# Optimization experiments

Measured on AMD Instinct MI355X. Metric: run time of the kernel, lower is better.

The kernel has to match this reference:

```python
import jax, jax.numpy as jnp
import numpy as np

NEG_SLOPE = 0.2
K_L = 0.5
K_G = 0.5
TEMP_G = 1e-3


def _leaky(v):
    return jnp.where(v >= 0, v, NEG_SLOPE * v)


def _topk_row_mask(scores, keep):
    # scores: [n, n, h]; torch.topk(dim=0) -> indices [keep, n] per head,
    # then head_mask[indices, :] = 1 selects whole ROWS (any column hit).
    n = scores.shape[0]
    s = jnp.transpose(scores, (1, 2, 0))        # [n_cols, h, n_rows]
    _, idx = jax.lax.top_k(s, keep)             # [n_cols, h, keep]

    def per_head(idx_h):                        # idx_h: [n_cols, keep]
        return jnp.zeros((n,), scores.dtype).at[idx_h.reshape(-1)].set(1.0)

    rows = jax.vmap(per_head, in_axes=1, out_axes=0)(idx)  # [h, n_rows]
    return jnp.transpose(rows)[:, None, :]      # [n_rows, 1, h] broadcast over cols


def setup_inputs() -> dict:
    key = jax.random.key(0)
    ks = jax.random.split(key, 8)
    n, in_f, feat_dim = 1024, 256, 128
    H, F = 4, 64                                # n_heads, n_hidden (out_features=256)
    feats = jax.random.normal(ks[0], (n, feat_dim), dtype=jnp.float32)
    x = jax.random.normal(ks[1], (n, in_f), dtype=jnp.float32)
    adj = jax.random.randint(ks[2], (n, n, 1), 0, 2).astype(jnp.int32)
    sc = 0.05
    W_l = jax.random.normal(ks[3], (in_f, H * F), dtype=jnp.float32) * sc
    W_r = jax.random.normal(ks[4], (in_f, H * F), dtype=jnp.float32) * sc
    attn_w = jax.random.normal(ks[5], (F,), dtype=jnp.float32) * sc
    W_delta = jax.random.normal(ks[6], (2 * F, F), dtype=jnp.float32) * sc
    b_delta = jnp.zeros((F,), dtype=jnp.float32)
    return {"feats": feats, "x": x, "adj": adj, "W_l": W_l, "W_r": W_r,
            "attn_w": attn_w, "W_delta": W_delta, "b_delta": b_delta}


def reference(feats, x, adj, W_l, W_r, attn_w, W_delta, b_delta):
    n = x.shape[0]
    F = attn_w.shape[0]
    H = W_l.shape[1] // F
    g_l = (x @ W_l).reshape(n, H, F)
    g_r = (x @ W_r).reshape(n, H, F)
    # g_sum[i, j] = g_l[j] + g_r[i]  (repeat vs repeat_interleave ordering)
    g_sum = g_r[:, None, :, :] + g_l[None, :, :, :]          # [n, n, H, F]
    e = jnp.einsum('ijhf,f->ijh', _leaky(g_sum), attn_w)     # [n, n, H]

    mask_adj = adj > 0                                        # [n, n, 1]
    a_l = jax.nn.softmax(jnp.where(mask_adj, e, -jnp.inf), axis=1)
    a_1nd = a_l * mask_adj.astype(e.dtype)

    keep_l = int(n * (1.0 - K_L))
    a_filt = a_1nd * _topk_row_mask(a_1nd, keep_l)
    attn_local = jnp.einsum('ijh,jhf->ihf', a_filt, g_r)     # [n, H, F]

    omega = jax.nn.softmax(e, axis=1)
    fn = (feats - feats.min(axis=0)) / (feats.max(axis=0) - feats.min(axis=0))
    fn = jnp.where(jnp.isnan(fn), 0.0, fn)
    g_rn = (g_r - g_r.min(axis=0)) / (g_r.max(axis=0) - g_r.min(axis=0))
    nf = jnp.linalg.norm(fn, axis=1)                          # [n] (index j)
    ng = jnp.linalg.norm(g_rn, axis=2)                        # [n, H] (index i)
    alpha = jax.nn.softmax(jnp.abs(nf[None, :, None] - ng[:, None, :]), axis=1)
    gamma = 0.5 * (omega + (1.0 - alpha))

    keep_g = int(n * (1.0 - K_G))
    gf = gamma * _topk_row_mask(gamma, keep_g)
    gf = jax.nn.softmax(jnp.where(gf == 0, 1e-10, gf) / TEMP_G, axis=1)
    attn_global = jnp.einsum('ijh,jhf->ihf', gf, g_r)         # [n, H, F]

    inter = _leaky(jnp.concatenate([attn_local, attn_global], axis=2) @ W_delta + b_delta)
    delta = jax.nn.softmax(inter, axis=1)                     # softmax over heads (torch dim=1)
    attn_res = delta * attn_local + (1.0 - delta) * attn_global
    return attn_res.reshape(n, H * F)
```

## Files before the change

kernel.cpp:

```cpp
#include <hip/hip_runtime.h>
#include <cstdint>
#include <cstddef>

#define N 1024
#define HN 4
#define FDIM 64
#define KSEL 512
#define FLT_MAX_ 3.402823466e+38f

__device__ __forceinline__ float wred_sum(float v){
#pragma unroll
  for(int o=32;o>0;o>>=1) v += __shfl_down(v,o,64);
  return v;
}
__device__ __forceinline__ float wred_max(float v){
#pragma unroll
  for(int o=32;o>0;o>>=1) v = fmaxf(v,__shfl_down(v,o,64));
  return v;
}
__device__ __forceinline__ float bred_sum(float v, float* scr){
  int t=threadIdx.x;
  v = wred_sum(v);
  __syncthreads();
  if((t&63)==0) scr[t>>6]=v;
  __syncthreads();
  return (scr[0]+scr[1])+(scr[2]+scr[3]);
}
__device__ __forceinline__ float bred_max(float v, float* scr){
  int t=threadIdx.x;
  v = wred_max(v);
  __syncthreads();
  if((t&63)==0) scr[t>>6]=v;
  __syncthreads();
  return fmaxf(fmaxf(scr[0],scr[1]),fmaxf(scr[2],scr[3]));
}

__global__ __launch_bounds__(256) void zero_ints(int* p, int n){
  int i = blockIdx.x*256 + threadIdx.x;
  if(i<n) p[i]=0;
}

__global__ __launch_bounds__(256) void gemm_lr(const float* __restrict__ x,
                                               const float* __restrict__ W_l,
                                               const float* __restrict__ W_r,
                                               float* __restrict__ g_l,
                                               float* __restrict__ g_r){
  int i0 = blockIdx.x*4, t = threadIdx.x;
  const float* __restrict__ W = blockIdx.y ? W_r : W_l;
  float* __restrict__ g = blockIdx.y ? g_r : g_l;
  float acc[4] = {0.f,0.f,0.f,0.f};
#pragma unroll 8
  for(int k=0;k<256;k++){
    float w = W[(size_t)k*256 + t];
#pragma unroll
    for(int r=0;r<4;r++) acc[r] = fmaf(x[(size_t)(i0+r)*256 + k], w, acc[r]);
  }
#pragma unroll
  for(int r=0;r<4;r++) g[(size_t)(i0+r)*256 + t] = acc[r];
}

__global__ __launch_bounds__(256) void colmm_part(const float* __restrict__ feats,
                                                  const float* __restrict__ g_r,
                                                  float* __restrict__ pmin_f, float* __restrict__ pmax_f,
                                                  float* __restrict__ pmin_g, float* __restrict__ pmax_g){
  int chunk = blockIdx.x, src = blockIdx.y, t = threadIdx.x;
  int cols = src ? 256 : 128;
  const float* in = src ? g_r : feats;
  if(t < cols){
    float lo = FLT_MAX_, hi = -FLT_MAX_;
    int r0 = chunk*64;
    for(int r=0;r<64;r++){
      float v = in[(size_t)(r0+r)*cols + t];
      lo = fminf(lo,v); hi = fmaxf(hi,v);
    }
    if(src){ pmin_g[chunk*256+t]=lo; pmax_g[chunk*256+t]=hi; }
    else   { pmin_f[chunk*128+t]=lo; pmax_f[chunk*128+t]=hi; }
  }
}

__global__ __launch_bounds__(256) void colmm_fin(const float* __restrict__ pmin_f, const float* __restrict__ pmax_f,
                                                 const float* __restrict__ pmin_g, const float* __restrict__ pmax_g,
                                                 float* __restrict__ fmn, float* __restrict__ fmx,
                                                 float* __restrict__ gmn, float* __restrict__ gmx){
  int src = blockIdx.x, t = threadIdx.x;
  int cols = src ? 256 : 128;
  if(t < cols){
    float lo = FLT_MAX_, hi = -FLT_MAX_;
    const float* pn = src ? pmin_g : pmin_f;
    const float* px = src ? pmax_g : pmax_f;
    for(int k=0;k<16;k++){
      lo = fminf(lo, pn[k*cols+t]);
      hi = fmaxf(hi, px[k*cols+t]);
    }
    if(src){ gmn[t]=lo; gmx[t]=hi; } else { fmn[t]=lo; fmx[t]=hi; }
  }
}

__global__ __launch_bounds__(256) void norms_kernel(const float* __restrict__ feats,
                                                    const float* __restrict__ g_r,
                                                    const float* __restrict__ fmn, const float* __restrict__ fmx,
                                                    const float* __restrict__ gmn, const float* __restrict__ gmx,
                                                    float* __restrict__ nf, float* __restrict__ ng){
  __shared__ float scr[4];
  int i = blockIdx.x, z = blockIdx.y, t = threadIdx.x;
  if(z==0){
    float u = 0.f;
    if(t < 128){
      float d = fmx[t]-fmn[t];
      float v = feats[(size_t)i*128 + t];
      u = (d==0.f) ? 0.f : (v - fmn[t])/d;
    }
    float tot = bred_sum(u*u, scr);
    if(t==0) nf[i] = sqrtf(tot);
  } else {
    int c = t, hh = t>>6;
    float d = gmx[c]-gmn[c];
    float v = g_r[(size_t)i*256 + c];
    float u = (v - gmn[c])/d;
    float ss = wred_sum(u*u);
    if((t&63)==0) ng[hh*N + i] = sqrtf(ss);
  }
}

__global__ __launch_bounds__(256) void compute_e(const float* __restrict__ g_l,
                                                 const float* __restrict__ g_r,
                                                 const float* __restrict__ attn_w,
                                                 float* __restrict__ e){
  __shared__ __align__(16) float grs[64][68];
  __shared__ __align__(16) float gls[64][68];
  __shared__ __align__(16) float aw[64], aw2[64];
  int h = blockIdx.z, i0 = blockIdx.y*64, j0 = blockIdx.x*64;
  int t = threadIdx.x;
  if(t < 64){ float w = attn_w[t]; aw[t]=w; aw2[t]=0.2f*w; }
#pragma unroll
  for(int k=0;k<16;k++){
    int idx = t + k*256; int r = idx>>6, f = idx&63;
    grs[r][f] = g_r[(size_t)(i0+r)*256 + h*64 + f];
    gls[r][f] = g_l[(size_t)(j0+r)*256 + h*64 + f];
  }
  __syncthreads();
  int tj = t&15, ti = t>>4;
  float acc[4][4];
#pragma unroll
  for(int a=0;a<4;a++)
#pragma unroll
    for(int b=0;b<4;b++) acc[a][b]=0.f;
  for(int fc=0; fc<64; fc+=4){
    float4 wv  = *(float4*)&aw[fc];
    float4 wv2 = *(float4*)&aw2[fc];
    float4 ga4[4], gb4[4];
#pragma unroll
    for(int a=0;a<4;a++) ga4[a] = *(float4*)&grs[ti*4+a][fc];
#pragma unroll
    for(int b=0;b<4;b++) gb4[b] = *(float4*)&gls[tj+16*b][fc];
#pragma unroll
    for(int a=0;a<4;a++)
#pragma unroll
      for(int b=0;b<4;b++){
        float s0 = ga4[a].x + gb4[b].x;
        float s1 = ga4[a].y + gb4[b].y;
        float s2 = ga4[a].z + gb4[b].z;
        float s3 = ga4[a].w + gb4[b].w;
        acc[a][b] = fmaf(s0, (s0>=0.f)?wv.x:wv2.x, acc[a][b]);
        acc[a][b] = fmaf(s1, (s1>=0.f)?wv.y:wv2.y, acc[a][b]);
        acc[a][b] = fmaf(s2, (s2>=0.f)?wv.z:wv2.z, acc[a][b]);
        acc[a][b] = fmaf(s3, (s3>=0.f)?wv.w:wv2.w, acc[a][b]);
      }
  }
#pragma unroll
  for(int a=0;a<4;a++)
#pragma unroll
    for(int b=0;b<4;b++){
      int i = i0 + ti*4 + a, j = j0 + tj + 16*b;
      e[((size_t)h*N + i)*N + j] = acc[a][b];
    }
}

__global__ __launch_bounds__(256) void row_stats(const float* __restrict__ e,
                                                 const int* __restrict__ adj,
                                                 const float* __restrict__ nf,
                                                 const float* __restrict__ ng,
                                                 float* __restrict__ mlA, float* __restrict__ islA,
                                                 float* __restrict__ moA, float* __restrict__ isoA,
                                                 float* __restrict__ maA, float* __restrict__ isaA,
                                                 float* __restrict__ mgA, float* __restrict__ sgA){
  __shared__ float es[1024];
  __shared__ float nfs[1024];
  __shared__ unsigned char adjs[1024];
  __shared__ float scr[4];
  int i = blockIdx.x, h = blockIdx.y, t = threadIdx.x;
  size_t base = ((size_t)h*N + i)*N;
  float ngv = ng[h*N + i];
#pragma unroll
  for(int k=0;k<4;k++){
    int j = t + k*256;
    es[j]  = e[base + j];
    nfs[j] = nf[j];
    adjs[j] = (adj[(size_t)i*N + j] > 0) ? 1 : 0;
  }
  __syncthreads();
  float ml=-FLT_MAX_, mo=-FLT_MAX_, ma=-FLT_MAX_;
#pragma unroll
  for(int k=0;k<4;k++){
    int j = t + k*256;
    float ev = es[j];
    mo = fmaxf(mo, ev);
    if(adjs[j]) ml = fmaxf(ml, ev);
    ma = fmaxf(ma, fabsf(nfs[j]-ngv));
  }
  ml = bred_max(ml, scr); mo = bred_max(mo, scr); ma = bred_max(ma, scr);
  float sl=0.f, so=0.f, sa=0.f;
#pragma unroll
  for(int k=0;k<4;k++){
    int j = t + k*256;
    float ev = es[j];
    so += __expf(ev-mo);
    if(adjs[j]) sl += __expf(ev-ml);
    sa += __expf(fabsf(nfs[j]-ngv)-ma);
  }
  sl = bred_sum(sl, scr); so = bred_sum(so, scr); sa = bred_sum(sa, scr);
  float isl = 1.f/sl, iso = 1.f/so, isa = 1.f/sa;
  float mg = -FLT_MAX_;
  float gloc[4];
#pragma unroll
  for(int k=0;k<4;k++){
    int j = t + k*256;
    float ev = es[j];
    float omega = __expf(ev-mo)*iso;
    float alpha = __expf(fabsf(nfs[j]-ngv)-ma)*isa;
    float g = 0.5f*(omega + 1.f - alpha);
    gloc[k] = g;
    mg = fmaxf(mg, g);
  }
  mg = bred_max(mg, scr);
  float sg = 0.f;
#pragma unroll
  for(int k=0;k<4;k++) sg += __expf((gloc[k]-mg)/1e-3f);
  sg = bred_sum(sg, scr);
  if(t==0){
    mlA[h*N+i]=ml; islA[h*N+i]=isl;
    moA[h*N+i]=mo; isoA[h*N+i]=iso;
    maA[h*N+i]=ma; isaA[h*N+i]=isa;
    mgA[h*N+i]=mg; sgA[h*N+i]=sg;
  }
}

__global__ __launch_bounds__(256) void applyT(float* __restrict__ e,
                                              float* __restrict__ gamT,
                                              const int* __restrict__ adj,
                                              const float* __restrict__ nf,
                                              const float* __restrict__ mlA, const float* __restrict__ islA,
                                              const float* __restrict__ moA, const float* __restrict__ isoA,
                                              const float* __restrict__ maA, const float* __restrict__ isaA,
                                              const float* __restrict__ ng){
  __shared__ __align__(16) float buf1[64][65];
  __shared__ __align__(16) float buf2[64][65];
  __shared__ __align__(16) float buf3[64][65];
  __shared__ float rml[64], risl[64], rmo[64], riso[64], rma[64], risa[64], rng[64], nfs[64];
  int h = blockIdx.y;
  int pp = blockIdx.x; int a = 0;
  while(pp >= 16 - a){ pp -= 16 - a; a++; }
  int b = a + pp;
  int t = threadIdx.x;
  int rg = t >> 4, c4 = t & 15;

  int i0 = a*64, j0 = b*64;
  if(t < 64){
    int o = h*N + i0 + t;
    rml[t]=mlA[o]; risl[t]=islA[o]; rmo[t]=moA[o]; riso[t]=isoA[o];
    rma[t]=maA[o]; risa[t]=isaA[o]; rng[t]=ng[o]; nfs[t]=nf[j0+t];
  }
  __syncthreads();
  float4 ev[4]; int4 av[4];
#pragma unroll
  for(int k=0;k<4;k++){
    int row = rg*4+k;
    ev[k] = *(const float4*)(e + ((size_t)h*N + i0+row)*N + j0 + c4*4);
    av[k] = *(const int4*)(adj + (size_t)(i0+row)*N + j0 + c4*4);
  }
#pragma unroll
  for(int k=0;k<4;k++){
    int row = rg*4+k;
    float ml=rml[row], isl=risl[row], mo=rmo[row], iso=riso[row];
    float ma=rma[row], isa=risa[row], ngv=rng[row];
    float evc[4] = {ev[k].x,ev[k].y,ev[k].z,ev[k].w};
    int   avc[4] = {av[k].x,av[k].y,av[k].z,av[k].w};
#pragma unroll
    for(int c=0;c<4;c++){
      int j = c4*4+c;
      buf2[j][row] = (avc[c]>0) ? __expf(evc[c]-ml)*isl : 0.f;
      float omega = __expf(evc[c]-mo)*iso;
      float alpha = __expf(fabsf(nfs[j]-ngv)-ma)*isa;
      buf1[j][row] = 0.5f*(omega + 1.f - alpha);
    }
  }
  __syncthreads();
#pragma unroll
  for(int k=0;k<4;k++){
    int jr = rg*4+k;
    *(float4*)(gamT + ((size_t)h*N + j0+jr)*N + i0 + c4*4) = *(float4*)&buf1[jr][c4*4];
  }
  if(a == b){
#pragma unroll
    for(int k=0;k<4;k++){
      int jr = rg*4+k;
      *(float4*)(e + ((size_t)h*N + j0+jr)*N + i0 + c4*4) = *(float4*)&buf2[jr][c4*4];
    }
    return;
  }
  int i1 = b*64, j1 = a*64;
  __syncthreads();
  if(t < 64){
    int o = h*N + i1 + t;
    rml[t]=mlA[o]; risl[t]=islA[o]; rmo[t]=moA[o]; riso[t]=isoA[o];
    rma[t]=maA[o]; risa[t]=isaA[o]; rng[t]=ng[o]; nfs[t]=nf[j1+t];
  }
#pragma unroll
  for(int k=0;k<4;k++){
    int row = rg*4+k;
    ev[k] = *(const float4*)(e + ((size_t)h*N + i1+row)*N + j1 + c4*4);
    av[k] = *(const int4*)(adj + (size_t)(i1+row)*N + j1 + c4*4);
  }
  __syncthreads();
#pragma unroll
  for(int k=0;k<4;k++){
    int jr = rg*4+k;
    *(float4*)(e + ((size_t)h*N + i1+jr)*N + j1 + c4*4) = *(float4*)&buf2[jr][c4*4];
  }
#pragma unroll
  for(int k=0;k<4;k++){
    int row = rg*4+k;
    float ml=rml[row], isl=risl[row], mo=rmo[row], iso=riso[row];
    float ma=rma[row], isa=risa[row], ngv=rng[row];
    float evc[4] = {ev[k].x,ev[k].y,ev[k].z,ev[k].w};
    int   avc[4] = {av[k].x,av[k].y,av[k].z,av[k].w};
#pragma unroll
    for(int c=0;c<4;c++){
      int j = c4*4+c;
      buf3[j][row] = (avc[c]>0) ? __expf(evc[c]-ml)*isl : 0.f;
      float omega = __expf(evc[c]-mo)*iso;
      float alpha = __expf(fabsf(nfs[j]-ngv)-ma)*isa;
      buf1[j][row] = 0.5f*(omega + 1.f - alpha);
    }
  }
  __syncthreads();
#pragma unroll
  for(int k=0;k<4;k++){
    int jr = rg*4+k;
    *(float4*)(gamT + ((size_t)h*N + j1+jr)*N + i1 + c4*4) = *(float4*)&buf1[jr][c4*4];
    *(float4*)(e    + ((size_t)h*N + j1+jr)*N + i1 + c4*4) = *(float4*)&buf3[jr][c4*4];
  }
}

__global__ __launch_bounds__(256) void colselect4(const float* __restrict__ a1T,
                                                  const float* __restrict__ gaT,
                                                  int* __restrict__ mask_l,
                                                  int* __restrict__ mask_g){
  __shared__ __align__(16) int hist[4][256];
  int t = threadIdx.x, w = t>>6, lane = t&63;
  int gcol = blockIdx.x*4 + w;
  int z  = gcol >> 12;
  int hj = gcol & 4095;
  int h  = hj >> 10;
  const float* __restrict__ src = (z ? gaT : a1T) + (size_t)hj * (size_t)N;
  int* __restrict__ mask = z ? mask_g : mask_l;
  int* hw = hist[w];

  unsigned ur[16];
#pragma unroll
  for(int c=0;c<4;c++){
    uint4 u4 = ((const uint4*)src)[c*64 + lane];
    ur[c*4+0]=u4.x; ur[c*4+1]=u4.y; ur[c*4+2]=u4.z; ur[c*4+3]=u4.w;
  }

  unsigned prefix = 0;
  int kth = KSEL, tiecnt = 0;
#pragma unroll
  for(int b=3;b>=0;b--){
    *(int4*)&hw[lane*4] = make_int4(0,0,0,0);
#pragma unroll
    for(int q=0;q<16;q++){
      unsigned u = ur[q];
      bool act = (b==3) || ((u >> (8*(b+1))) == prefix);
      if(act){
        int bucket = (u >> (8*b)) & 0xFF;
        unsigned long long mball = __ballot(true);
        int lead = __ffsll(mball) - 1;
        int maj = __shfl(bucket, lead, 64);
        if(bucket == maj){
          int cnt = (int)__popcll(__ballot(true));
          if(lane == lead) atomicAdd(&hw[maj], cnt);
        } else {
          atomicAdd(&hw[bucket], 1);
        }
      }
    }
    int4 hv = *(int4*)&hw[lane*4];
    int s = hv.x+hv.y+hv.z+hv.w;
    int P = s;
#pragma unroll
    for(int off=1; off<64; off<<=1){
      int q2 = __shfl_up(P, off, 64);
      if(lane >= off) P += q2;
    }
    int total = __shfl(P, 63, 64);
    int suffChunk  = total - (P - s);
    int suffChunkN = total - P;
    bool cross = (suffChunk >= kth) && (suffChunkN < kth);
    int selb=0, newk=0, tcnt=0;
    if(cross){
      int s3 = suffChunkN + hv.w;
      int s2 = s3 + hv.z;
      int s1 = s2 + hv.y;
      if(s3 >= kth){ selb=4*lane+3; newk = kth - suffChunkN; tcnt=hv.w; }
      else if(s2 >= kth){ selb=4*lane+2; newk = kth - s3; tcnt=hv.z; }
      else if(s1 >= kth){ selb=4*lane+1; newk = kth - s2; tcnt=hv.y; }
      else { selb=4*lane; newk = kth - s1; tcnt=hv.x; }
    }
    unsigned long long cm = __ballot(cross);
    int csrc = __ffsll(cm) - 1;
    selb   = __shfl(selb, csrc, 64);
    kth    = __shfl(newk, csrc, 64);
    tiecnt = __shfl(tcnt, csrc, 64);
    prefix = (prefix << 8) | (unsigned)selb;
  }

  unsigned T = prefix;
  int tneed = kth;
  if(tiecnt == tneed){
#pragma unroll
    for(int c=0;c<4;c++)
#pragma unroll
      for(int k2=0;k2<4;k2++){
        int i = c*256 + lane*4 + k2;
        if(ur[c*4+k2] >= T) mask[h*N + i] = 1;
      }
  } else {
    int base = 0;
#pragma unroll
    for(int c=0;c<4;c++){
      int tc=0;
#pragma unroll
      for(int k2=0;k2<4;k2++) tc += (ur[c*4+k2]==T)?1:0;
      int pc = tc;
#pragma unroll
      for(int off=1; off<64; off<<=1){
        int q2 = __shfl_up(pc, off, 64);
        if(lane >= off) pc += q2;
      }
      int ctot = __shfl(pc, 63, 64);
      int run = base + pc - tc;
#pragma unroll
      for(int k2=0;k2<4;k2++){
        int i = c*256 + lane*4 + k2;
        unsigned u = ur[c*4+k2];
        bool sel = (u > T) || (u == T && run < tneed);
        run += (u==T)?1:0;
        if(sel) mask[h*N + i] = 1;
      }
      base += ctot;
    }
  }
}

__global__ __launch_bounds__(256) void attn_mm(const float* __restrict__ a1T,
                                               const float* __restrict__ gaT,
                                               const float* __restrict__ g_r,
                                               const float* __restrict__ mgA,
                                               const float* __restrict__ sgA,
                                               const int* __restrict__ mask_g,
                                               float* __restrict__ partL,
                                               float* __restrict__ partG){
  __shared__ __align__(16) float a_t[32][68];
  __shared__ __align__(16) float p_t[32][68];
  __shared__ __align__(16) float b_s[32][68];
  __shared__ float mgv[64], isgv[64];
  __shared__ int mgf[64];
  int i0 = blockIdx.x*64, h = blockIdx.y, s = blockIdx.z, j0 = s*128;
  int t = threadIdx.x;
  if(t < 64){
    mgv[t]  = mgA[h*N + i0 + t];
    isgv[t] = 1.f / sgA[h*N + i0 + t];
    mgf[t]  = mask_g[h*N + i0 + t];
  }
  __syncthreads();
  int fq = t & 15, iq = t >> 4;
  float4 accL[4], accG[4];
#pragma unroll
  for(int r=0;r<4;r++){ accL[r]=make_float4(0,0,0,0); accG[r]=make_float4(0,0,0,0); }
  for(int sub=0; sub<4; sub++){
    int jb = j0 + sub*32;
#pragma unroll
    for(int k=0;k<2;k++){
      int idx = t + k*256;
      int jj = idx>>4, i4 = idx&15;
      size_t base = ((size_t)h*N + jb + jj)*N + i0 + i4*4;
      *(float4*)&a_t[jj][i4*4] = *(const float4*)(a1T + base);
      float4 g4 = *(const float4*)(gaT + base);
      int ii = i4*4;
      const float inv = 1.f/1024.f;
      float4 p4;
      p4.x = mgf[ii+0] ? __expf((g4.x - mgv[ii+0])/1e-3f)*isgv[ii+0] : inv;
      p4.y = mgf[ii+1] ? __expf((g4.y - mgv[ii+1])/1e-3f)*isgv[ii+1] : inv;
      p4.z = mgf[ii+2] ? __expf((g4.z - mgv[ii+2])/1e-3f)*isgv[ii+2] : inv;
      p4.w = mgf[ii+3] ? __expf((g4.w - mgv[ii+3])/1e-3f)*isgv[ii+3] : inv;
      *(float4*)&p_t[jj][i4*4] = p4;
      *(float4*)&b_s[jj][i4*4] = *(const float4*)(g_r + (size_t)(jb+jj)*256 + h*64 + i4*4);
    }
    __syncthreads();
#pragma unroll 4
    for(int j=0;j<32;j++){
      float4 bv = *(float4*)&b_s[j][fq*4];
      float4 av = *(float4*)&a_t[j][iq*4];
      float4 pv = *(float4*)&p_t[j][iq*4];
      accL[0].x = fmaf(av.x, bv.x, accL[0].x); accL[0].y = fmaf(av.x, bv.y, accL[0].y);
      accL[0].z = fmaf(av.x, bv.z, accL[0].z); accL[0].w = fmaf(av.x, bv.w, accL[0].w);
      accL[1].x = fmaf(av.y, bv.x, accL[1].x); accL[1].y = fmaf(av.y, bv.y, accL[1].y);
      accL[1].z = fmaf(av.y, bv.z, accL[1].z); accL[1].w = fmaf(av.y, bv.w, accL[1].w);
      accL[2].x = fmaf(av.z, bv.x, accL[2].x); accL[2].y = fmaf(av.z, bv.y, accL[2].y);
      accL[2].z = fmaf(av.z, bv.z, accL[2].z); accL[2].w = fmaf(av.z, bv.w, accL[2].w);
      accL[3].x = fmaf(av.w, bv.x, accL[3].x); accL[3].y = fmaf(av.w, bv.y, accL[3].y);
      accL[3].z = fmaf(av.w, bv.z, accL[3].z); accL[3].w = fmaf(av.w, bv.w, accL[3].w);
      accG[0].x = fmaf(pv.x, bv.x, accG[0].x); accG[0].y = fmaf(pv.x, bv.y, accG[0].y);
      accG[0].z = fmaf(pv.x, bv.z, accG[0].z); accG[0].w = fmaf(pv.x, bv.w, accG[0].w);
      accG[1].x = fmaf(pv.y, bv.x, accG[1].x); accG[1].y = fmaf(pv.y, bv.y, accG[1].y);
      accG[1].z = fmaf(pv.y, bv.z, accG[1].z); accG[1].w = fmaf(pv.y, bv.w, accG[1].w);
      accG[2].x = fmaf(pv.z, bv.x, accG[2].x); accG[2].y = fmaf(pv.z, bv.y, accG[2].y);
      accG[2].z = fmaf(pv.z, bv.z, accG[2].z); accG[2].w = fmaf(pv.z, bv.w, accG[2].w);
      accG[3].x = fmaf(pv.w, bv.x, accG[3].x); accG[3].y = fmaf(pv.w, bv.y, accG[3].y);
      accG[3].z = fmaf(pv.w, bv.z, accG[3].z); accG[3].w = fmaf(pv.w, bv.w, accG[3].w);
    }
    __syncthreads();
  }
#pragma unroll
  for(int r=0;r<4;r++){
    int i = i0 + iq*4 + r;
    size_t o = ((size_t)s*N + i)*256 + h*64 + fq*4;
    *(float4*)&partL[o] = accL[r];
    *(float4*)&partG[o] = accG[r];
  }
}

__global__ __launch_bounds__(256) void epilogue(const float* __restrict__ partL,
                                                const float* __restrict__ partG,
                                                const int* __restrict__ mask_l,
                                                const float* __restrict__ W_delta,
                                                const float* __restrict__ b_delta,
                                                float* __restrict__ out){
  __shared__ float cat[4][128];
  __shared__ float inter_s[4][64];
  int i = blockIdx.x, t = threadIdx.x;
  int h = t>>6, f = t&63;
  float sl = 0.f, sg = 0.f;
#pragma unroll
  for(int s2=0;s2<8;s2++){
    size_t o = ((size_t)s2*N + i)*256 + h*64 + f;
    sl += partL[o];
    sg += partG[o];
  }
  if(!mask_l[h*N + i]) sl = 0.f;
  cat[h][f]      = sl;
  cat[h][64 + f] = sg;
  __syncthreads();
  float d = b_delta[f];
  for(int c=0;c<128;c++) d = fmaf(cat[h][c], W_delta[(size_t)c*64 + f], d);
  d = (d >= 0.f) ? d : 0.2f*d;
  inter_s[h][f] = d;
  __syncthreads();
  float m = inter_s[0][f];
#pragma unroll
  for(int hh=1;hh<4;hh++) m = fmaxf(m, inter_s[hh][f]);
  float ssum = 0.f;
#pragma unroll
  for(int hh=0;hh<4;hh++) ssum += __expf(inter_s[hh][f]-m);
  float delta = __expf(d - m)/ssum;
  out[(size_t)i*256 + h*64 + f] = delta*sl + (1.f - delta)*sg;
}

extern "C" void kernel_launch(void* const* d_in, const int* in_sizes, int n_in,
                              void* d_out, int out_size, void* d_ws, size_t ws_size,
                              hipStream_t stream) {
  const float* feats  = (const float*)d_in[0];
  const float* x      = (const float*)d_in[1];
  const int*   adj    = (const int*)  d_in[2];
  const float* W_l    = (const float*)d_in[3];
  const float* W_r    = (const float*)d_in[4];
  const float* attn_w = (const float*)d_in[5];
  const float* W_delta= (const float*)d_in[6];
  const float* b_delta= (const float*)d_in[7];
  float* out = (float*)d_out;

  float* ws = (float*)d_ws;
  size_t off = 0;
  float* g_l   = ws+off; off += (size_t)N*256;
  float* g_r   = ws+off; off += (size_t)N*256;
  float* e     = ws+off; off += (size_t)HN*N*N;
  float* gam   = ws+off; off += (size_t)HN*N*N;
  float* partL = ws+off; off += (size_t)8*N*256;
  float* partG = ws+off; off += (size_t)8*N*256;
  float* pmin_f= ws+off; off += 16*128;
  float* pmax_f= ws+off; off += 16*128;
  float* pmin_g= ws+off; off += 16*256;
  float* pmax_g= ws+off; off += 16*256;
  float* fmn   = ws+off; off += 128;
  float* fmx   = ws+off; off += 128;
  float* gmn   = ws+off; off += 256;
  float* gmx   = ws+off; off += 256;
  float* nf    = ws+off; off += N;
  float* ng    = ws+off; off += (size_t)HN*N;
  float* mlA   = ws+off; off += (size_t)HN*N;
  float* islA  = ws+off; off += (size_t)HN*N;
  float* moA   = ws+off; off += (size_t)HN*N;
  float* isoA  = ws+off; off += (size_t)HN*N;
  float* maA   = ws+off; off += (size_t)HN*N;
  float* isaA  = ws+off; off += (size_t)HN*N;
  float* mgA   = ws+off; off += (size_t)HN*N;
  float* sgA   = ws+off; off += (size_t)HN*N;
  int* mask_l  = (int*)(ws+off); off += (size_t)HN*N;
  int* mask_g  = (int*)(ws+off); off += (size_t)HN*N;

  zero_ints<<<32, 256, 0, stream>>>(mask_l, 2*HN*N);

  gemm_lr<<<dim3(256,2), 256, 0, stream>>>(x, W_l, W_r, g_l, g_r);

  colmm_part<<<dim3(16,2), 256, 0, stream>>>(feats, g_r, pmin_f, pmax_f, pmin_g, pmax_g);
  colmm_fin <<<dim3(2),    256, 0, stream>>>(pmin_f, pmax_f, pmin_g, pmax_g, fmn, fmx, gmn, gmx);
  norms_kernel<<<dim3(N,2),256, 0, stream>>>(feats, g_r, fmn, fmx, gmn, gmx, nf, ng);

  compute_e<<<dim3(16,16,HN), 256, 0, stream>>>(g_l, g_r, attn_w, e);

  row_stats<<<dim3(N,HN), 256, 0, stream>>>(e, adj, nf, ng, mlA, islA, moA, isoA, maA, isaA, mgA, sgA);

  applyT<<<dim3(136,HN), 256, 0, stream>>>(e, gam, adj, nf, mlA, islA, moA, isoA, maA, isaA, ng);

  colselect4<<<2048, 256, 0, stream>>>(e, gam, mask_l, mask_g);

  attn_mm<<<dim3(16,HN,8), 256, 0, stream>>>(e, gam, g_r, mgA, sgA, mask_g, partL, partG);

  epilogue<<<N, 256, 0, stream>>>(partL, partG, mask_l, W_delta, b_delta, out);
}
```

Measured before the change: 218.7 us.

## Bit-pack adjacency, use one wave per row in row_stats, skip zeros in radix select

A new pack_adj kernel turns the int32 adjacency matrix into bitmasks once and also zeroes the masks, replacing zero_ints. row_stats and applyT then read the bitmask instead of the full int matrix. row_stats now handles one row per wavefront for all four heads, keeping values in registers and using butterfly shuffles in place of shared-memory block reductions. The column radix select counts nonzero entries first, skips the histogram passes when fewer than KSEL are positive, and iterates only over active nonzero elements. This cuts adjacency memory traffic and block barriers, at the cost of an extra full read of adj in the packing kernel and more divergent loops in the select.

```diff
diff --git a/kernel.cpp b/kernel.cpp
--- a/kernel.cpp
+++ b/kernel.cpp
@@ -13,9 +13,19 @@
   for(int o=32;o>0;o>>=1) v += __shfl_down(v,o,64);
   return v;
 }
-__device__ __forceinline__ float wred_max(float v){
-#pragma unroll
-  for(int o=32;o>0;o>>=1) v = fmaxf(v,__shfl_down(v,o,64));
+__device__ __forceinline__ float bfly_sum(float v){
+#pragma unroll
+  for(int o=1;o<64;o<<=1) v += __shfl_xor(v,o,64);
+  return v;
+}
+__device__ __forceinline__ float bfly_max(float v){
+#pragma unroll
+  for(int o=1;o<64;o<<=1) v = fmaxf(v,__shfl_xor(v,o,64));
+  return v;
+}
+__device__ __forceinline__ int bfly_sumi(int v){
+#pragma unroll
+  for(int o=1;o<64;o<<=1) v += __shfl_xor(v,o,64);
   return v;
 }
 __device__ __forceinline__ float bred_sum(float v, float* scr){
@@ -26,18 +36,22 @@
   __syncthreads();
   return (scr[0]+scr[1])+(scr[2]+scr[3]);
 }
-__device__ __forceinline__ float bred_max(float v, float* scr){
-  int t=threadIdx.x;
-  v = wred_max(v);
-  __syncthreads();
-  if((t&63)==0) scr[t>>6]=v;
-  __syncthreads();
-  return fmaxf(fmaxf(scr[0],scr[1]),fmaxf(scr[2],scr[3]));
-}
-
-__global__ __launch_bounds__(256) void zero_ints(int* p, int n){
-  int i = blockIdx.x*256 + threadIdx.x;
-  if(i<n) p[i]=0;
+
+__global__ __launch_bounds__(256) void pack_adj(const int* __restrict__ adj,
+                                                unsigned* __restrict__ adjbit,
+                                                int* __restrict__ masks){
+  int i = blockIdx.x, t = threadIdx.x, w = t>>6, lane = t&63;
+  if(i < 32) masks[i*256 + t] = 0;
+#pragma unroll
+  for(int it=0; it<4; it++){
+    int j = w*256 + it*64 + lane;
+    int v = adj[(size_t)i*N + j];
+    unsigned long long mb = __ballot(v > 0);
+    if(lane == 0){
+      adjbit[i*32 + w*8 + it*2]     = (unsigned)mb;
+      adjbit[i*32 + w*8 + it*2 + 1] = (unsigned)(mb >> 32);
+    }
+  }
 }
 
 __global__ __launch_bounds__(256) void gemm_lr(const float* __restrict__ x,
@@ -177,67 +191,68 @@
 }
 
 __global__ __launch_bounds__(256) void row_stats(const float* __restrict__ e,
-                                                 const int* __restrict__ adj,
+                                                 const unsigned* __restrict__ adjbit,
                                                  const float* __restrict__ nf,
                                                  const float* __restrict__ ng,
                                                  float* __restrict__ mlA, float* __restrict__ islA,
                                                  float* __restrict__ moA, float* __restrict__ isoA,
                                                  float* __restrict__ maA, float* __restrict__ isaA,
                                                  float* __restrict__ mgA, float* __restrict__ sgA){
-  __shared__ float es[1024];
-  __shared__ float nfs[1024];
-  __shared__ unsigned char adjs[1024];
-  __shared__ float scr[4];
-  int i = blockIdx.x, h = blockIdx.y, t = threadIdx.x;
+  int i = blockIdx.x, t = threadIdx.x, h = t>>6, lane = t&63;
   size_t base = ((size_t)h*N + i)*N;
+  float er[16], nfr[16];
+  unsigned nib[4];
+#pragma unroll
+  for(int c=0;c<4;c++){
+    float4 e4 = *(const float4*)(e  + base + c*256 + lane*4);
+    float4 n4 = *(const float4*)(nf + c*256 + lane*4);
+    er[c*4+0]=e4.x; er[c*4+1]=e4.y; er[c*4+2]=e4.z; er[c*4+3]=e4.w;
+    nfr[c*4+0]=n4.x; nfr[c*4+1]=n4.y; nfr[c*4+2]=n4.z; nfr[c*4+3]=n4.w;
+    nib[c] = (adjbit[i*32 + c*8 + (lane>>3)] >> ((lane&7)*4)) & 0xFu;
+  }
   float ngv = ng[h*N + i];
-#pragma unroll
-  for(int k=0;k<4;k++){
-    int j = t + k*256;
-    es[j]  = e[base + j];
-    nfs[j] = nf[j];
-    adjs[j] = (adj[(size_t)i*N + j] > 0) ? 1 : 0;
-  }
-  __syncthreads();
   float ml=-FLT_MAX_, mo=-FLT_MAX_, ma=-FLT_MAX_;
 #pragma unroll
-  for(int k=0;k<4;k++){
-    int j = t + k*256;
-    float ev = es[j];
-    mo = fmaxf(mo, ev);
-    if(adjs[j]) ml = fmaxf(ml, ev);
-    ma = fmaxf(ma, fabsf(nfs[j]-ngv));
-  }
-  ml = bred_max(ml, scr); mo = bred_max(mo, scr); ma = bred_max(ma, scr);
+  for(int c=0;c<4;c++)
+#pragma unroll
+    for(int k=0;k<4;k++){
+      int q = c*4+k;
+      float ev = er[q];
+      mo = fmaxf(mo, ev);
+      if((nib[c]>>k)&1) ml = fmaxf(ml, ev);
+      ma = fmaxf(ma, fabsf(nfr[q]-ngv));
+    }
+  ml = bfly_max(ml); mo = bfly_max(mo); ma = bfly_max(ma);
   float sl=0.f, so=0.f, sa=0.f;
 #pragma unroll
-  for(int k=0;k<4;k++){
-    int j = t + k*256;
-    float ev = es[j];
-    so += __expf(ev-mo);
-    if(adjs[j]) sl += __expf(ev-ml);
-    sa += __expf(fabsf(nfs[j]-ngv)-ma);
-  }
-  sl = bred_sum(sl, scr); so = bred_sum(so, scr); sa = bred_sum(sa, scr);
+  for(int c=0;c<4;c++)
+#pragma unroll
+    for(int k=0;k<4;k++){
+      int q = c*4+k;
+      float ev = er[q];
+      so += __expf(ev-mo);
+      if((nib[c]>>k)&1) sl += __expf(ev-ml);
+      sa += __expf(fabsf(nfr[q]-ngv)-ma);
+    }
+  sl = bfly_sum(sl); so = bfly_sum(so); sa = bfly_sum(sa);
   float isl = 1.f/sl, iso = 1.f/so, isa = 1.f/sa;
+  float gg[16];
   float mg = -FLT_MAX_;
-  float gloc[4];
-#pragma unroll
-  for(int k=0;k<4;k++){
-    int j = t + k*256;
-    float ev = es[j];
+#pragma unroll
+  for(int q=0;q<16;q++){
+    float ev = er[q];
     float omega = __expf(ev-mo)*iso;
-    float alpha = __expf(fabsf(nfs[j]-ngv)-ma)*isa;
+    float alpha = __expf(fabsf(nfr[q]-ngv)-ma)*isa;
     float g = 0.5f*(omega + 1.f - alpha);
-    gloc[k] = g;
+    gg[q] = g;
     mg = fmaxf(mg, g);
   }
-  mg = bred_max(mg, scr);
+  mg = bfly_max(mg);
   float sg = 0.f;
 #pragma unroll
-  for(int k=0;k<4;k++) sg += __expf((gloc[k]-mg)/1e-3f);
-  sg = bred_sum(sg, scr);
-  if(t==0){
+  for(int q=0;q<16;q++) sg += __expf((gg[q]-mg)/1e-3f);
+  sg = bfly_sum(sg);
+  if(lane==0){
     mlA[h*N+i]=ml; islA[h*N+i]=isl;
     moA[h*N+i]=mo; isoA[h*N+i]=iso;
     maA[h*N+i]=ma; isaA[h*N+i]=isa;
@@ -247,7 +262,7 @@
 
 __global__ __launch_bounds__(256) void applyT(float* __restrict__ e,
                                               float* __restrict__ gamT,
-                                              const int* __restrict__ adj,
+                                              const unsigned* __restrict__ adjbit,
                                               const float* __restrict__ nf,
                                               const float* __restrict__ mlA, const float* __restrict__ islA,
                                               const float* __restrict__ moA, const float* __restrict__ isoA,
@@ -271,12 +286,12 @@
     rma[t]=maA[o]; risa[t]=isaA[o]; rng[t]=ng[o]; nfs[t]=nf[j0+t];
   }
   __syncthreads();
-  float4 ev[4]; int4 av[4];
+  float4 ev[4]; unsigned nb[4];
 #pragma unroll
   for(int k=0;k<4;k++){
     int row = rg*4+k;
     ev[k] = *(const float4*)(e + ((size_t)h*N + i0+row)*N + j0 + c4*4);
-    av[k] = *(const int4*)(adj + (size_t)(i0+row)*N + j0 + c4*4);
+    nb[k] = (adjbit[(size_t)(i0+row)*32 + (j0>>5) + (c4>>3)] >> ((c4&7)*4)) & 0xFu;
   }
 #pragma unroll
   for(int k=0;k<4;k++){
@@ -284,11 +299,10 @@
     float ml=rml[row], isl=risl[row], mo=rmo[row], iso=riso[row];
     float ma=rma[row], isa=risa[row], ngv=rng[row];
     float evc[4] = {ev[k].x,ev[k].y,ev[k].z,ev[k].w};
-    int   avc[4] = {av[k].x,av[k].y,av[k].z,av[k].w};
 #pragma unroll
     for(int c=0;c<4;c++){
       int j = c4*4+c;
-      buf2[j][row] = (avc[c]>0) ? __expf(evc[c]-ml)*isl : 0.f;
+      buf2[j][row] = ((nb[k]>>c)&1) ? __expf(evc[c]-ml)*isl : 0.f;
       float omega = __expf(evc[c]-mo)*iso;
       float alpha = __expf(fabsf(nfs[j]-ngv)-ma)*isa;
       buf1[j][row] = 0.5f*(omega + 1.f - alpha);
@@ -319,7 +333,7 @@
   for(int k=0;k<4;k++){
     int row = rg*4+k;
     ev[k] = *(const float4*)(e + ((size_t)h*N + i1+row)*N + j1 + c4*4);
-    av[k] = *(const int4*)(adj + (size_t)(i1+row)*N + j1 + c4*4);
+    nb[k] = (adjbit[(size_t)(i1+row)*32 + (j1>>5) + (c4>>3)] >> ((c4&7)*4)) & 0xFu;
   }
   __syncthreads();
 #pragma unroll
@@ -333,11 +347,10 @@
     float ml=rml[row], isl=risl[row], mo=rmo[row], iso=riso[row];
     float ma=rma[row], isa=risa[row], ngv=rng[row];
     float evc[4] = {ev[k].x,ev[k].y,ev[k].z,ev[k].w};
-    int   avc[4] = {av[k].x,av[k].y,av[k].z,av[k].w};
 #pragma unroll
     for(int c=0;c<4;c++){
       int j = c4*4+c;
-      buf3[j][row] = (avc[c]>0) ? __expf(evc[c]-ml)*isl : 0.f;
+      buf3[j][row] = ((nb[k]>>c)&1) ? __expf(evc[c]-ml)*isl : 0.f;
       float omega = __expf(evc[c]-mo)*iso;
       float alpha = __expf(fabsf(nfs[j]-ngv)-ma)*isa;
       buf1[j][row] = 0.5f*(omega + 1.f - alpha);
@@ -352,7 +365,7 @@
   }
 }
 
-__global__ __launch_bounds__(256) void colselect4(const float* __restrict__ a1T,
+__global__ __launch_bounds__(256) void colselect5(const float* __restrict__ a1T,
                                                   const float* __restrict__ gaT,
                                                   int* __restrict__ mask_l,
                                                   int* __restrict__ mask_g){
@@ -372,61 +385,85 @@
     uint4 u4 = ((const uint4*)src)[c*64 + lane];
     ur[c*4+0]=u4.x; ur[c*4+1]=u4.y; ur[c*4+2]=u4.z; ur[c*4+3]=u4.w;
   }
-
-  unsigned prefix = 0;
-  int kth = KSEL, tiecnt = 0;
-#pragma unroll
-  for(int b=3;b>=0;b--){
+  unsigned pm = 0;
+#pragma unroll
+  for(int q=0;q<16;q++) if(ur[q] != 0u) pm |= (1u<<q);
+  int cnt_pos = bfly_sumi(__popc(pm));
+
+  unsigned T; int tneed; int tiecnt = -1;
+  if(cnt_pos < KSEL){
+    T = 0u; tneed = KSEL - cnt_pos;
+  } else {
+    unsigned am = pm;
+    unsigned prefix = 0; int kth = KSEL;
     *(int4*)&hw[lane*4] = make_int4(0,0,0,0);
-#pragma unroll
-    for(int q=0;q<16;q++){
-      unsigned u = ur[q];
-      bool act = (b==3) || ((u >> (8*(b+1))) == prefix);
-      if(act){
-        int bucket = (u >> (8*b)) & 0xFF;
-        unsigned long long mball = __ballot(true);
-        int lead = __ffsll(mball) - 1;
+    {
+      unsigned m = am;
+      while(m){
+        int q = __ffs(m)-1; m &= m-1;
+        int bucket = (int)(ur[q] >> 24);
+        unsigned long long mb = __ballot(true);
+        int lead = __ffsll(mb) - 1;
         int maj = __shfl(bucket, lead, 64);
         if(bucket == maj){
           int cnt = (int)__popcll(__ballot(true));
           if(lane == lead) atomicAdd(&hw[maj], cnt);
-        } else {
-          atomicAdd(&hw[bucket], 1);
+        } else atomicAdd(&hw[bucket], 1);
+      }
+    }
+#pragma unroll
+    for(int b=3;b>=0;b--){
+      if(b < 3){
+        *(int4*)&hw[lane*4] = make_int4(0,0,0,0);
+        unsigned m = am;
+        int shf = 8*(b+1);
+        while(m){
+          int q = __ffs(m)-1; m &= m-1;
+          unsigned u = ur[q];
+          if((u >> shf) == prefix){
+            int bucket = (int)((u >> (8*b)) & 0xFF);
+            unsigned long long mb = __ballot(true);
+            int lead = __ffsll(mb) - 1;
+            int maj = __shfl(bucket, lead, 64);
+            if(bucket == maj){
+              int cnt = (int)__popcll(__ballot(true));
+              if(lane == lead) atomicAdd(&hw[maj], cnt);
+            } else atomicAdd(&hw[bucket], 1);
+          } else am &= ~(1u<<q);
         }
       }
-    }
-    int4 hv = *(int4*)&hw[lane*4];
-    int s = hv.x+hv.y+hv.z+hv.w;
-    int P = s;
-#pragma unroll
-    for(int off=1; off<64; off<<=1){
-      int q2 = __shfl_up(P, off, 64);
-      if(lane >= off) P += q2;
-    }
-    int total = __shfl(P, 63, 64);
-    int suffChunk  = total - (P - s);
-    int suffChunkN = total - P;
-    bool cross = (suffChunk >= kth) && (suffChunkN < kth);
-    int selb=0, newk=0, tcnt=0;
-    if(cross){
-      int s3 = suffChunkN + hv.w;
-      int s2 = s3 + hv.z;
-      int s1 = s2 + hv.y;
-      if(s3 >= kth){ selb=4*lane+3; newk = kth - suffChunkN; tcnt=hv.w; }
-      else if(s2 >= kth){ selb=4*lane+2; newk = kth - s3; tcnt=hv.z; }
-      else if(s1 >= kth){ selb=4*lane+1; newk = kth - s2; tcnt=hv.y; }
-      else { selb=4*lane; newk = kth - s1; tcnt=hv.x; }
-    }
-    unsigned long long cm = __ballot(cross);
-    int csrc = __ffsll(cm) - 1;
-    selb   = __shfl(selb, csrc, 64);
-    kth    = __shfl(newk, csrc, 64);
-    tiecnt = __shfl(tcnt, csrc, 64);
-    prefix = (prefix << 8) | (unsigned)selb;
-  }
-
-  unsigned T = prefix;
-  int tneed = kth;
+      int4 hv = *(int4*)&hw[lane*4];
+      int s = hv.x+hv.y+hv.z+hv.w;
+      int P = s;
+#pragma unroll
+      for(int off=1; off<64; off<<=1){
+        int q2 = __shfl_up(P, off, 64);
+        if(lane >= off) P += q2;
+      }
+      int total = __shfl(P, 63, 64);
+      int suffChunk  = total - (P - s);
+      int suffChunkN = total - P;
+      bool cross = (suffChunk >= kth) && (suffChunkN < kth);
+      int selb=0, newk=0, tcnt=0;
+      if(cross){
+        int s3 = suffChunkN + hv.w;
+        int s2 = s3 + hv.z;
+        int s1 = s2 + hv.y;
+        if(s3 >= kth){ selb=4*lane+3; newk = kth - suffChunkN; tcnt=hv.w; }
+        else if(s2 >= kth){ selb=4*lane+2; newk = kth - s3; tcnt=hv.z; }
+        else if(s1 >= kth){ selb=4*lane+1; newk = kth - s2; tcnt=hv.y; }
+        else { selb=4*lane; newk = kth - s1; tcnt=hv.x; }
+      }
+      unsigned long long cm = __ballot(cross);
+      int csrc = __ffsll(cm) - 1;
+      selb   = __shfl(selb, csrc, 64);
+      kth    = __shfl(newk, csrc, 64);
+      tiecnt = __shfl(tcnt, csrc, 64);
+      prefix = (prefix << 8) | (unsigned)selb;
+    }
+    T = prefix; tneed = kth;
+  }
+
   if(tiecnt == tneed){
 #pragma unroll
     for(int c=0;c<4;c++)
@@ -618,8 +655,9 @@
   float* sgA   = ws+off; off += (size_t)HN*N;
   int* mask_l  = (int*)(ws+off); off += (size_t)HN*N;
   int* mask_g  = (int*)(ws+off); off += (size_t)HN*N;
-
-  zero_ints<<<32, 256, 0, stream>>>(mask_l, 2*HN*N);
+  unsigned* adjbit = (unsigned*)(ws+off); off += (size_t)N*32;
+
+  pack_adj<<<N, 256, 0, stream>>>(adj, adjbit, mask_l);
 
   gemm_lr<<<dim3(256,2), 256, 0, stream>>>(x, W_l, W_r, g_l, g_r);
 
@@ -629,11 +667,11 @@
 
   compute_e<<<dim3(16,16,HN), 256, 0, stream>>>(g_l, g_r, attn_w, e);
 
-  row_stats<<<dim3(N,HN), 256, 0, stream>>>(e, adj, nf, ng, mlA, islA, moA, isoA, maA, isaA, mgA, sgA);
-
-  applyT<<<dim3(136,HN), 256, 0, stream>>>(e, gam, adj, nf, mlA, islA, moA, isoA, maA, isaA, ng);
-
-  colselect4<<<2048, 256, 0, stream>>>(e, gam, mask_l, mask_g);
+  row_stats<<<N, 256, 0, stream>>>(e, adjbit, nf, ng, mlA, islA, moA, isoA, maA, isaA, mgA, sgA);
+
+  applyT<<<dim3(136,HN), 256, 0, stream>>>(e, gam, adjbit, nf, mlA, islA, moA, isoA, maA, isaA, ng);
+
+  colselect5<<<2048, 256, 0, stream>>>(e, gam, mask_l, mask_g);
 
   attn_mm<<<dim3(16,HN,8), 256, 0, stream>>>(e, gam, g_r, mgA, sgA, mask_g, partL, partG);
 
```

After: 219.8 us. Within noise of the previous version (+0.5%).
